# Performance work log

Hardware: AMD Instinct MI355X
Metric: run time of the kernel (lower is better)

The kernel has to match this reference:

```python
import jax, jax.numpy as jnp
import numpy as np

B, N, T, D, H = 8, 64, 512, 128, 7


def setup_inputs() -> dict:
    key = jax.random.key(0)
    k1, k2, k3 = jax.random.split(key, 3)
    ego = jax.random.normal(k1, (B, T, D), dtype=jnp.float32)
    others = jax.random.normal(k2, (B, N, T, D), dtype=jnp.float32)
    queries = jax.random.normal(k3, (H, D), dtype=jnp.float32)
    return {"ego": ego, "others": others, "queries": queries}


def reference(ego, others, queries):
    # ego: (B,T,D) -- only its shape is used in the original module
    # others: (B,N,T,D); queries: (H,D)
    d = queries.shape[-1]
    scale = d ** (-0.5)
    # logits: (B,T,H,N) -- batched GEMM instead of broadcasted mul+sum
    logits = jnp.einsum('bntd,hd->bthn', others, queries) * scale
    weights = jax.nn.softmax(logits, axis=-1)
    # ctx: (B,T,H,D)
    ctx = jnp.einsum('bthn,bntd->bthd', weights, others)
    return ctx
```

## Files before the change

### kernel.cpp

```cpp
#include <hip/hip_runtime.h>
#include <hip/hip_bf16.h>

#define B_ 8
#define N_ 64
#define T_ 512
#define D_ 128
#define H_ 7

typedef __attribute__((ext_vector_type(8))) short short8;
typedef __attribute__((ext_vector_type(4))) float f32x4;
typedef __attribute__((ext_vector_type(4))) int   iv4;

union BF2 { __hip_bfloat162 h2; unsigned u; };
__device__ __forceinline__ unsigned pk2(float a, float b) {
    BF2 r; r.h2 = __float22bfloat162_rn(make_float2(a, b)); return r.u;
}
__device__ __forceinline__ short8 cvt8(const float4& a, const float4& b) {
    iv4 v = { (int)pk2(a.x, a.y), (int)pk2(a.z, a.w),
              (int)pk2(b.x, b.y), (int)pk2(b.z, b.w) };
    return __builtin_bit_cast(short8, v);
}

__global__ __launch_bounds__(256, 8)
void MultiHeadPool_45226005627089_kernel(const float* __restrict__ others,
                                         const float* __restrict__ queries,
                                         float* __restrict__ out) {
    __shared__ __align__(16) ushort XL[N_ * 136];
    __shared__ __align__(16) ushort WL[16 * 72];
    __shared__ __align__(16) float  SM[16 * 4];

    const int tid = threadIdx.x;
    const int w   = tid >> 6;
    const int l   = tid & 63;
    const int c   = l & 15;
    const int p   = l >> 4;

    const int bt = blockIdx.x;
    const int b  = bt >> 9;
    const int t  = bt & (T_ - 1);

    const float* obase = others + ((size_t)b * N_ * T_ + t) * D_;
    const int    n     = 16 * w + c;
    const float* xrow  = obase + (size_t)n * (T_ * D_);
    const int    swn   = ((n >> 3) & 3) << 4;

    short8 xb[4];
    {
        float4 t0 = *(const float4*)(xrow + 8 * p);
        float4 t1 = *(const float4*)(xrow + 8 * p + 4);
        float4 t2 = *(const float4*)(xrow + 32 + 8 * p);
        float4 t3 = *(const float4*)(xrow + 32 + 8 * p + 4);
        xb[0] = cvt8(t0, t1);
        xb[1] = cvt8(t2, t3);
        t0 = *(const float4*)(xrow + 64 + 8 * p);
        t1 = *(const float4*)(xrow + 64 + 8 * p + 4);
        t2 = *(const float4*)(xrow + 96 + 8 * p);
        t3 = *(const float4*)(xrow + 96 + 8 * p + 4);
        xb[2] = cvt8(t0, t1);
        xb[3] = cvt8(t2, t3);
    }
    #pragma unroll
    for (int s = 0; s < 4; ++s) {
        const int d0 = (32 * s + 8 * p) ^ swn;
        *(short8*)&XL[n * 136 + d0] = xb[s];
    }

    short8 qb[4];
    {
        const float* qrow = queries + (c < H_ ? c : 0) * D_;
        #pragma unroll
        for (int s = 0; s < 4; ++s) {
            const float4 a  = *(const float4*)(qrow + 32 * s + 8 * p);
            const float4 bq = *(const float4*)(qrow + 32 * s + 8 * p + 4);
            qb[s] = cvt8(a, bq);
        }
    }

    f32x4 c1 = {0.f, 0.f, 0.f, 0.f};
    #pragma unroll
    for (int s = 0; s < 4; ++s)
        c1 = __builtin_amdgcn_mfma_f32_16x16x32_bf16(xb[s], qb[s], c1, 0, 0, 0);

    const float scale = 0.0883883476483184f;
    float e[4];
    #pragma unroll
    for (int r = 0; r < 4; ++r) e[r] = __expf(c1[r] * scale);
    float s_w = e[0] + e[1] + e[2] + e[3];
    s_w += __shfl_xor(s_w, 16);
    s_w += __shfl_xor(s_w, 32);
    if (l < 16) SM[c * 4 + w] = s_w;

    {
        const unsigned w01 = pk2(e[0], e[1]);
        const unsigned w23 = pk2(e[2], e[3]);
        *(uint2*)&WL[c * 72 + 16 * w + 4 * p] = make_uint2(w01, w23);
    }
    __syncthreads();

    short8 a2[2];
    #pragma unroll
    for (int ks = 0; ks < 2; ++ks)
        a2[ks] = *(const short8*)&WL[c * 72 + 32 * ks + 8 * p];

    f32x4 o2[2];
    #pragma unroll
    for (int dti = 0; dti < 2; ++dti) {
        const int dt = 2 * w + dti;
        f32x4 acc = {0.f, 0.f, 0.f, 0.f};
        #pragma unroll
        for (int ks = 0; ks < 2; ++ks) {
            const int base = (32 * ks + 8 * p) * 136 + ((16 * dt + c) ^ (p << 4));
            short8 bf;
            #pragma unroll
            for (int jj = 0; jj < 8; ++jj)
                bf[jj] = (short)XL[base + 136 * jj];
            acc = __builtin_amdgcn_mfma_f32_16x16x32_bf16(a2[ks], bf, acc, 0, 0, 0);
        }
        o2[dti] = acc;
    }

    float rz[4];
    #pragma unroll
    for (int r = 0; r < 4; ++r) {
        const int h = 4 * p + r;
        const float4 z4 = *(const float4*)&SM[h * 4];
        rz[r] = 1.0f / (z4.x + z4.y + z4.z + z4.w);
    }

    #pragma unroll
    for (int dti = 0; dti < 2; ++dti) {
        const int d = 16 * (2 * w + dti) + c;
        #pragma unroll
        for (int r = 0; r < 4; ++r) {
            const int h = 4 * p + r;
            if (h < H_)
                out[(size_t)bt * (H_ * D_) + h * D_ + d] = o2[dti][r] * rz[r];
        }
    }
}

extern "C" void kernel_launch(void* const* d_in, const int* in_sizes, int n_in,
                              void* d_out, int out_size, void* d_ws, size_t ws_size,
                              hipStream_t stream) {
    const float* others  = (const float*)d_in[1];
    const float* queries = (const float*)d_in[2];
    float* out = (float*)d_out;

    dim3 grid(B_ * T_);
    dim3 block(256);
    MultiHeadPool_45226005627089_kernel<<<grid, block, 0, stream>>>(others, queries, out);
}
```

Measured before the change: 32.58 us.

## Process two timesteps per block with register prefetch of next tile

Each block now handles two consecutive t values instead of one, halving the grid. The second timestep's rows are loaded into registers while the first is being processed, overlapping global load latency with compute. The queries conversion is also amortized over two timesteps. In exchange it adds an extra barrier per iteration, raises register pressure (launch bounds lowered to 6), and leaves fewer blocks to spread across CUs.

```diff
diff --git a/kernel.cpp b/kernel.cpp
--- a/kernel.cpp
+++ b/kernel.cpp
@@ -21,7 +21,7 @@
     return __builtin_bit_cast(short8, v);
 }
 
-__global__ __launch_bounds__(256, 8)
+__global__ __launch_bounds__(256, 6)
 void MultiHeadPool_45226005627089_kernel(const float* __restrict__ others,
                                          const float* __restrict__ queries,
                                          float* __restrict__ out) {
@@ -35,35 +35,15 @@
     const int c   = l & 15;
     const int p   = l >> 4;
 
-    const int bt = blockIdx.x;
-    const int b  = bt >> 9;
-    const int t  = bt & (T_ - 1);
+    const int blk = blockIdx.x;
+    const int b   = blk >> 8;
+    const int t0  = (blk & 255) * 2;
 
-    const float* obase = others + ((size_t)b * N_ * T_ + t) * D_;
-    const int    n     = 16 * w + c;
-    const float* xrow  = obase + (size_t)n * (T_ * D_);
-    const int    swn   = ((n >> 3) & 3) << 4;
-
-    short8 xb[4];
-    {
-        float4 t0 = *(const float4*)(xrow + 8 * p);
-        float4 t1 = *(const float4*)(xrow + 8 * p + 4);
-        float4 t2 = *(const float4*)(xrow + 32 + 8 * p);
-        float4 t3 = *(const float4*)(xrow + 32 + 8 * p + 4);
-        xb[0] = cvt8(t0, t1);
-        xb[1] = cvt8(t2, t3);
-        t0 = *(const float4*)(xrow + 64 + 8 * p);
-        t1 = *(const float4*)(xrow + 64 + 8 * p + 4);
-        t2 = *(const float4*)(xrow + 96 + 8 * p);
-        t3 = *(const float4*)(xrow + 96 + 8 * p + 4);
-        xb[2] = cvt8(t0, t1);
-        xb[3] = cvt8(t2, t3);
-    }
-    #pragma unroll
-    for (int s = 0; s < 4; ++s) {
-        const int d0 = (32 * s + 8 * p) ^ swn;
-        *(short8*)&XL[n * 136 + d0] = xb[s];
-    }
+    const int    n    = 16 * w + c;
+    const int    swn  = ((n >> 3) & 3) << 4;
+    const float* xrow = others + ((size_t)b * N_ * T_ + t0) * D_
+                               + (size_t)n * (T_ * D_) + 8 * p;
+    float* obt = out + ((size_t)(b * T_ + t0)) * (H_ * D_);
 
     short8 qb[4];
     {
@@ -76,66 +56,91 @@
         }
     }
 
-    f32x4 c1 = {0.f, 0.f, 0.f, 0.f};
+    float4 pre[8];
     #pragma unroll
-    for (int s = 0; s < 4; ++s)
-        c1 = __builtin_amdgcn_mfma_f32_16x16x32_bf16(xb[s], qb[s], c1, 0, 0, 0);
-
-    const float scale = 0.0883883476483184f;
-    float e[4];
-    #pragma unroll
-    for (int r = 0; r < 4; ++r) e[r] = __expf(c1[r] * scale);
-    float s_w = e[0] + e[1] + e[2] + e[3];
-    s_w += __shfl_xor(s_w, 16);
-    s_w += __shfl_xor(s_w, 32);
-    if (l < 16) SM[c * 4 + w] = s_w;
-
-    {
-        const unsigned w01 = pk2(e[0], e[1]);
-        const unsigned w23 = pk2(e[2], e[3]);
-        *(uint2*)&WL[c * 72 + 16 * w + 4 * p] = make_uint2(w01, w23);
-    }
-    __syncthreads();
-
-    short8 a2[2];
-    #pragma unroll
-    for (int ks = 0; ks < 2; ++ks)
-        a2[ks] = *(const short8*)&WL[c * 72 + 32 * ks + 8 * p];
-
-    f32x4 o2[2];
-    #pragma unroll
-    for (int dti = 0; dti < 2; ++dti) {
-        const int dt = 2 * w + dti;
-        f32x4 acc = {0.f, 0.f, 0.f, 0.f};
-        #pragma unroll
-        for (int ks = 0; ks < 2; ++ks) {
-            const int base = (32 * ks + 8 * p) * 136 + ((16 * dt + c) ^ (p << 4));
-            short8 bf;
-            #pragma unroll
-            for (int jj = 0; jj < 8; ++jj)
-                bf[jj] = (short)XL[base + 136 * jj];
-            acc = __builtin_amdgcn_mfma_f32_16x16x32_bf16(a2[ks], bf, acc, 0, 0, 0);
-        }
-        o2[dti] = acc;
+    for (int s = 0; s < 4; ++s) {
+        pre[2 * s]     = *(const float4*)(xrow + 32 * s);
+        pre[2 * s + 1] = *(const float4*)(xrow + 32 * s + 4);
     }
 
-    float rz[4];
-    #pragma unroll
-    for (int r = 0; r < 4; ++r) {
-        const int h = 4 * p + r;
-        const float4 z4 = *(const float4*)&SM[h * 4];
-        rz[r] = 1.0f / (z4.x + z4.y + z4.z + z4.w);
-    }
+    for (int it = 0; it < 2; ++it) {
+        short8 xb[4];
+        #pragma unroll
+        for (int s = 0; s < 4; ++s) {
+            xb[s] = cvt8(pre[2 * s], pre[2 * s + 1]);
+            const int d0 = (32 * s + 8 * p) ^ swn;
+            *(short8*)&XL[n * 136 + d0] = xb[s];
+        }
 
-    #pragma unroll
-    for (int dti = 0; dti < 2; ++dti) {
-        const int d = 16 * (2 * w + dti) + c;
+        if (it == 0) {
+            #pragma unroll
+            for (int s = 0; s < 4; ++s) {
+                pre[2 * s]     = *(const float4*)(xrow + D_ + 32 * s);
+                pre[2 * s + 1] = *(const float4*)(xrow + D_ + 32 * s + 4);
+            }
+        }
+
+        f32x4 c1 = {0.f, 0.f, 0.f, 0.f};
+        #pragma unroll
+        for (int s = 0; s < 4; ++s)
+            c1 = __builtin_amdgcn_mfma_f32_16x16x32_bf16(xb[s], qb[s], c1, 0, 0, 0);
+
+        const float scale = 0.0883883476483184f;
+        float e[4];
+        #pragma unroll
+        for (int r = 0; r < 4; ++r) e[r] = __expf(c1[r] * scale);
+        float s_w = e[0] + e[1] + e[2] + e[3];
+        s_w += __shfl_xor(s_w, 16);
+        s_w += __shfl_xor(s_w, 32);
+        if (l < 16) SM[c * 4 + w] = s_w;
+        {
+            const unsigned w01 = pk2(e[0], e[1]);
+            const unsigned w23 = pk2(e[2], e[3]);
+            *(uint2*)&WL[c * 72 + 16 * w + 4 * p] = make_uint2(w01, w23);
+        }
+        __syncthreads();
+
+        short8 a2[2];
+        #pragma unroll
+        for (int ks = 0; ks < 2; ++ks)
+            a2[ks] = *(const short8*)&WL[c * 72 + 32 * ks + 8 * p];
+
+        f32x4 o2[2];
+        #pragma unroll
+        for (int dti = 0; dti < 2; ++dti) {
+            const int dt = 2 * w + dti;
+            f32x4 acc = {0.f, 0.f, 0.f, 0.f};
+            #pragma unroll
+            for (int ks = 0; ks < 2; ++ks) {
+                const int base = (32 * ks + 8 * p) * 136 + ((16 * dt + c) ^ (p << 4));
+                short8 bf;
+                #pragma unroll
+                for (int jj = 0; jj < 8; ++jj)
+                    bf[jj] = (short)XL[base + 136 * jj];
+                acc = __builtin_amdgcn_mfma_f32_16x16x32_bf16(a2[ks], bf, acc, 0, 0, 0);
+            }
+            o2[dti] = acc;
+        }
+
+        float rz[4];
         #pragma unroll
         for (int r = 0; r < 4; ++r) {
             const int h = 4 * p + r;
-            if (h < H_)
-                out[(size_t)bt * (H_ * D_) + h * D_ + d] = o2[dti][r] * rz[r];
+            const float4 z4 = *(const float4*)&SM[h * 4];
+            rz[r] = 1.0f / (z4.x + z4.y + z4.z + z4.w);
         }
+
+        #pragma unroll
+        for (int dti = 0; dti < 2; ++dti) {
+            const int d = 16 * (2 * w + dti) + c;
+            #pragma unroll
+            for (int r = 0; r < 4; ++r) {
+                const int h = 4 * p + r;
+                if (h < H_)
+                    obt[(size_t)it * (H_ * D_) + h * D_ + d] = o2[dti][r] * rz[r];
+            }
+        }
+        __syncthreads();
     }
 }
 
@@ -146,7 +151,7 @@
     const float* queries = (const float*)d_in[2];
     float* out = (float*)d_out;
 
-    dim3 grid(B_ * T_);
+    dim3 grid(B_ * T_ / 2);
     dim3 block(256);
     MultiHeadPool_45226005627089_kernel<<<grid, block, 0, stream>>>(others, queries, out);
 }
```

Result: slower. 35.28 us (+8.3%).
